# Optimization experiments

Measured on AMD Instinct MI355X. Metric: run time of the kernel, lower is better.

Reference implementation:

```python
import jax, jax.numpy as jnp
import numpy as np

N_NODES = 20000
STEPS = 10  # message_passing_steps


def _mlp(x, p):
    # 3-layer MLP: Linear->ReLU->Linear->ReLU->Linear (no final activation)
    W1, b1, W2, b2, W3, b3 = p
    h = jax.nn.relu(x @ W1 + b1)
    h = jax.nn.relu(h @ W2 + b2)
    return h @ W3 + b3


def _aggregate(dst, edge_attr, num_nodes):
    # scatter_add of edge features into destination nodes, degree-normalized (deg clamped to >=1)
    agg = jax.ops.segment_sum(edge_attr, dst, num_segments=num_nodes)
    deg = jax.ops.segment_sum(jnp.ones((dst.shape[0], 1), edge_attr.dtype), dst, num_segments=num_nodes)
    return agg / jnp.maximum(deg, 1.0)


def setup_inputs() -> dict:
    key = jax.random.key(0)
    N, EM, EC = N_NODES, 120000, 20000
    ND, MD, CD, OD, L = 12, 7, 4, 3, 128
    keys = iter(jax.random.split(key, 128))

    def lin(i, o):
        return (jax.random.normal(next(keys), (i, o), jnp.float32) * 0.05,
                jax.random.normal(next(keys), (o,), jnp.float32) * 0.05)

    inp = {
        "node_x": jax.random.normal(next(keys), (N, ND), jnp.float32),
        "mesh_edge_attr": jax.random.normal(next(keys), (EM, MD), jnp.float32),
        "contact_edge_attr": jax.random.normal(next(keys), (EC, CD), jnp.float32),
    }
    dims = {"ne": (ND, L), "me": (MD, L), "ce": (CD, L), "pe": (3 * L, L), "pn": (3 * L, L), "de": (L, OD)}
    for name, (i, o) in dims.items():
        W1, b1 = lin(i, L)
        W2, b2 = lin(L, L)
        W3, b3 = lin(L, o)
        for pn, p in zip(["W1", "b1", "W2", "b2", "W3", "b3"], [W1, b1, W2, b2, W3, b3]):
            inp[name + "_" + pn] = p
    inp["mesh_edge_index"] = jax.random.randint(next(keys), (2, EM), 0, N)
    inp["contact_edge_index"] = jax.random.randint(next(keys), (2, EC), 0, N)
    return inp


def reference(node_x, mesh_edge_attr, contact_edge_attr,
              ne_W1, ne_b1, ne_W2, ne_b2, ne_W3, ne_b3,
              me_W1, me_b1, me_W2, me_b2, me_W3, me_b3,
              ce_W1, ce_b1, ce_W2, ce_b2, ce_W3, ce_b3,
              pe_W1, pe_b1, pe_W2, pe_b2, pe_W3, pe_b3,
              pn_W1, pn_b1, pn_W2, pn_b2, pn_W3, pn_b3,
              de_W1, de_b1, de_W2, de_b2, de_W3, de_b3,
              mesh_edge_index, contact_edge_index):
    ne = (ne_W1, ne_b1, ne_W2, ne_b2, ne_W3, ne_b3)
    mep = (me_W1, me_b1, me_W2, me_b2, me_W3, me_b3)
    cep = (ce_W1, ce_b1, ce_W2, ce_b2, ce_W3, ce_b3)
    pe = (pe_W1, pe_b1, pe_W2, pe_b2, pe_W3, pe_b3)
    pn = (pn_W1, pn_b1, pn_W2, pn_b2, pn_W3, pn_b3)
    de = (de_W1, de_b1, de_W2, de_b2, de_W3, de_b3)
    N = node_x.shape[0]
    # encode
    x = _mlp(node_x, ne)                 # [N, 128]
    me = _mlp(mesh_edge_attr, mep)       # [EM, 128]
    ce = _mlp(contact_edge_attr, cep)    # [EC, 128]
    msrc, mdst = mesh_edge_index[0], mesh_edge_index[1]
    csrc, cdst = contact_edge_index[0], contact_edge_index[1]
    # process (shared edge_mlp for both edge types, residual updates)
    for _ in range(STEPS):
        me = me + _mlp(jnp.concatenate([x[msrc], x[mdst], me], axis=-1), pe)
        ce = ce + _mlp(jnp.concatenate([x[csrc], x[cdst], ce], axis=-1), pe)
        agg_m = _aggregate(mdst, me, N)
        agg_c = _aggregate(cdst, ce, N)
        x = x + _mlp(jnp.concatenate([x, agg_m, agg_c], axis=-1), pn)
    # decode
    return _mlp(x, de)                   # [N, 3]
```

## Files before the change

### kernel.cpp

```cpp
#include <hip/hip_runtime.h>
#include <stdint.h>

typedef unsigned short u16;
typedef __attribute__((ext_vector_type(8))) short bf16x8;
typedef __attribute__((ext_vector_type(4))) float f32x4;

#define NNODES 20000
#define EM 120000
#define EC 20000
#define LDIM 128
#define MT 32
#define MT2 64
#define A_STR 392
#define H_STR 136
#define G_STR 264

__device__ __forceinline__ u16 f2bf(float f){
  uint32_t b = __float_as_uint(f);
  b += 0x7FFF + ((b >> 16) & 1);
  return (u16)(b >> 16);
}

__device__ __forceinline__ f32x4 mfma16(bf16x8 a, bf16x8 b, f32x4 c){
  return __builtin_amdgcn_mfma_f32_16x16x32_bf16(a, b, c, 0, 0, 0);
}

template<int KB>
__device__ __forceinline__ void layer(const u16* sIn, int in_str, const u16* Wp,
                                      int wr, int wc, int lane, f32x4 acc[4]){
  const int row = wr*16 + (lane & 15);
  const int kg  = lane >> 4;
  #pragma unroll
  for (int kb = 0; kb < KB; ++kb){
    bf16x8 a = *(const bf16x8*)(sIn + row*in_str + kb*32 + kg*8);
    const u16* wb = Wp + (((kb*8 + wc*4)*64 + lane) << 3);
    #pragma unroll
    for (int nf = 0; nf < 4; ++nf){
      bf16x8 b = *(const bf16x8*)(wb + (nf << 9));
      acc[nf] = mfma16(a, b, acc[nf]);
    }
  }
}

__device__ __forceinline__ void hid_epi(f32x4 acc[4], const float* bias,
                                        int wr, int wc, int lane, u16* sOut){
  const int cl = lane & 15;
  const int r0 = wr*16 + (lane >> 4)*4;
  #pragma unroll
  for (int nf = 0; nf < 4; ++nf){
    int col = wc*64 + nf*16 + cl;
    float bv = bias[col];
    #pragma unroll
    for (int r = 0; r < 4; ++r){
      float v = acc[nf][r] + bv;
      sOut[(r0 + r)*H_STR + col] = f2bf(v > 0.f ? v : 0.f);
    }
  }
}

__device__ __forceinline__ void zero4(f32x4 acc[4]){
  const f32x4 vz = {0.f, 0.f, 0.f, 0.f};
  #pragma unroll
  for (int i = 0; i < 4; ++i) acc[i] = vz;
}

template<int KB, int STR>
__device__ __forceinline__ void layer64(const u16* sIn, const u16* Wp,
                                        int wr, int wc, int lane, f32x4 acc[2][2]){
  const int r0 = wr*32 + (lane & 15);
  const int kg = lane >> 4;
  const u16* a0p = sIn + r0*STR + kg*8;
  const u16* a1p = a0p + 16*STR;
  const u16* wb  = Wp + (((wc*2)*64 + lane) << 3);
  #pragma unroll
  for (int kb = 0; kb < KB; ++kb){
    bf16x8 a0 = *(const bf16x8*)(a0p + kb*32);
    bf16x8 a1 = *(const bf16x8*)(a1p + kb*32);
    const u16* wk = wb + kb*4096;
    bf16x8 b0 = *(const bf16x8*)(wk);
    bf16x8 b1 = *(const bf16x8*)(wk + 512);
    acc[0][0] = mfma16(a0, b0, acc[0][0]);
    acc[1][0] = mfma16(a1, b0, acc[1][0]);
    acc[0][1] = mfma16(a0, b1, acc[0][1]);
    acc[1][1] = mfma16(a1, b1, acc[1][1]);
  }
}

template<int STR>
__device__ __forceinline__ void hid_epi64(f32x4 acc[2][2], const float* bias,
                                          int wr, int wc, int lane, u16* sOut){
  const int cl = lane & 15;
  const int rq = (lane >> 4)*4;
  #pragma unroll
  for (int rf = 0; rf < 2; ++rf){
    int r0 = wr*32 + rf*16 + rq;
    #pragma unroll
    for (int nf = 0; nf < 2; ++nf){
      int col = wc*32 + nf*16 + cl;
      float bv = bias[col];
      #pragma unroll
      for (int r = 0; r < 4; ++r){
        float v = acc[rf][nf][r] + bv;
        sOut[(r0 + r)*STR + col] = f2bf(v > 0.f ? v : 0.f);
      }
    }
  }
}

__device__ __forceinline__ void zero22(f32x4 acc[2][2]){
  const f32x4 vz = {0.f, 0.f, 0.f, 0.f};
  acc[0][0] = vz; acc[0][1] = vz; acc[1][0] = vz; acc[1][1] = vz;
}

struct PackDesc { const float* src; int K_raw, N_raw, NF, elem_off; };
struct PackArgs { PackDesc d[18]; int total; };

__global__ __launch_bounds__(256) void pack_weights(PackArgs pa, u16* dst){
  int idx = blockIdx.x*256 + threadIdx.x;
  if (idx >= pa.total) return;
  int di = 0;
  #pragma unroll
  for (int i = 1; i < 18; ++i) if (idx >= pa.d[i].elem_off) di = i;
  PackDesc dd = pa.d[di];
  int e = idx - dd.elem_off;
  int f = e >> 9, lane = (e >> 3) & 63, j = e & 7;
  int kb = f / dd.NF, nf = f % dd.NF;
  int k = kb*32 + (lane >> 4)*8 + j;
  int n = nf*16 + (lane & 15);
  float v = (k < dd.K_raw && n < dd.N_raw) ? dd.src[k*dd.N_raw + n] : 0.f;
  dst[idx] = f2bf(v);
}

__global__ __launch_bounds__(256) void hist_kernel(const int* mdst, const int* cdst,
                                                   int* cnt_m, int* cnt_c){
  int i = blockIdx.x*256 + threadIdx.x;
  if (i < EM) atomicAdd(&cnt_m[mdst[i]], 1);
  else if (i < EM + EC) atomicAdd(&cnt_c[cdst[i - EM]], 1);
}

struct ScanArgs { const int *cnt_m, *cnt_c; int *start_m, *start_c, *cur_m, *cur_c; };

__global__ __launch_bounds__(256) void scan_kernel(ScanArgs a){
  const int n = NNODES;
  const int* cnt = blockIdx.x == 0 ? a.cnt_m : a.cnt_c;
  int* start     = blockIdx.x == 0 ? a.start_m : a.start_c;
  int* cur       = blockIdx.x == 0 ? a.cur_m : a.cur_c;
  __shared__ int part[256];
  __shared__ int base[257];
  int t = threadIdx.x;
  const int per = (n + 255) / 256;
  int lo = t*per, hi = min(n, lo + per);
  int s = 0;
  for (int j = lo; j < hi; ++j) s += cnt[j];
  part[t] = s;
  __syncthreads();
  if (t == 0){
    int run = 0;
    for (int i = 0; i < 256; ++i){ base[i] = run; run += part[i]; }
    base[256] = run;
  }
  __syncthreads();
  int run = base[t];
  for (int j = lo; j < hi; ++j){ start[j] = run; cur[j] = run; run += cnt[j]; }
  if (t == 255) start[n] = base[256];
}

__global__ __launch_bounds__(256) void scatter_kernel(const int* mdst, const int* cdst,
                                                      int* cur_m, int* cur_c,
                                                      int* eid_m, int* eid_c){
  int i = blockIdx.x*256 + threadIdx.x;
  if (i < EM){
    int p = atomicAdd(&cur_m[mdst[i]], 1);
    eid_m[p] = i;
  } else if (i < EM + EC){
    int e = i - EM;
    int p = atomicAdd(&cur_c[cdst[e]], 1);
    eid_c[p] = e;
  }
}

struct EncArgs {
  const float* in; int Kraw;
  const u16 *Wp1, *Wp2, *Wp3;
  const float *b1, *b2, *b3;
  float* out_f32; u16* out_b16;
};

__global__ __launch_bounds__(256) void enc_kernel(EncArgs a){
  __shared__ u16 sA[MT*A_STR];
  __shared__ u16 sH[MT*H_STR];
  const int tid = threadIdx.x, lane = tid & 63, w = tid >> 6, wr = w & 1, wc = w >> 1;
  const int m0 = blockIdx.x * MT;
  for (int i = tid; i < MT*32; i += 256){
    int row = i >> 5, c = i & 31;
    float v = (c < a.Kraw) ? a.in[(size_t)(m0 + row)*a.Kraw + c] : 0.f;
    sA[row*A_STR + c] = f2bf(v);
  }
  __syncthreads();
  f32x4 acc[4]; zero4(acc);
  layer<1>(sA, A_STR, a.Wp1, wr, wc, lane, acc);
  hid_epi(acc, a.b1, wr, wc, lane, sH);
  __syncthreads();
  zero4(acc);
  layer<4>(sH, H_STR, a.Wp2, wr, wc, lane, acc);
  hid_epi(acc, a.b2, wr, wc, lane, sA);
  __syncthreads();
  zero4(acc);
  layer<4>(sA, H_STR, a.Wp3, wr, wc, lane, acc);
  const int cl = lane & 15, r0l = wr*16 + (lane >> 4)*4;
  #pragma unroll
  for (int nf = 0; nf < 4; ++nf){
    int col = wc*64 + nf*16 + cl;
    float bv = a.b3[col];
    #pragma unroll
    for (int r = 0; r < 4; ++r){
      int m = m0 + r0l + r;
      float v = acc[nf][r] + bv;
      a.out_f32[(size_t)m*LDIM + col] = v;
      if (a.out_b16) a.out_b16[(size_t)m*LDIM + col] = f2bf(v);
    }
  }
}

struct EdgeArgs {
  const u16 *Wp1, *Wp2, *Wp3;
  const float *b1, *b2, *b3;
  const u16* x_b16;
  const int *msrc, *mdst, *csrc, *cdst;
  float *me_f32, *ce_f32;
  int mesh_blocks;
};

__global__ __launch_bounds__(512, 8) void edge_kernel(EdgeArgs a){
  __shared__ u16 sB0[MT2*H_STR];
  __shared__ u16 sB1[MT2*H_STR];
  const int tid = threadIdx.x, lane = tid & 63, w = tid >> 6, wr = w & 1, wc = w >> 1;
  const bool mesh = (int)blockIdx.x < a.mesh_blocks;
  const int e0 = (mesh ? (int)blockIdx.x : (int)blockIdx.x - a.mesh_blocks) * MT2;
  const int E = mesh ? EM : EC;
  const int* src = mesh ? a.msrc : a.csrc;
  const int* dst = mesh ? a.mdst : a.cdst;
  float* ff = mesh ? a.me_f32 : a.ce_f32;

  const int r0 = wr*32 + (lane & 15);
  int eA = e0 + r0;      if (eA >= E) eA = E - 1;
  int eB = e0 + r0 + 16; if (eB >= E) eB = E - 1;
  const int sA_ = src[eA], sB_ = src[eB], dA_ = dst[eA], dB_ = dst[eB];

  #pragma unroll
  for (int t = tid; t < MT2*16; t += 512){
    int row = t >> 4, ch = t & 15;
    int e = e0 + row; if (e >= E) e = E - 1;
    const float* sp = ff + (size_t)e*LDIM + ch*8;
    bf16x8 v;
    #pragma unroll
    for (int j = 0; j < 8; ++j) v[j] = (short)f2bf(sp[j]);
    *(bf16x8*)(sB0 + row*H_STR + ch*8) = v;
  }
  __syncthreads();

  f32x4 acc[2][2]; zero22(acc);
  {
    const int cb = (lane >> 4)*8;
    const u16* wb = a.Wp1 + (((wc*2)*64 + lane) << 3);
    #pragma unroll
    for (int kb = 0; kb < 12; ++kb){
      bf16x8 a0, a1;
      if (kb < 4){
        a0 = *(const bf16x8*)(a.x_b16 + (size_t)sA_*LDIM + kb*32 + cb);
        a1 = *(const bf16x8*)(a.x_b16 + (size_t)sB_*LDIM + kb*32 + cb);
      } else if (kb < 8){
        a0 = *(const bf16x8*)(a.x_b16 + (size_t)dA_*LDIM + (kb-4)*32 + cb);
        a1 = *(const bf16x8*)(a.x_b16 + (size_t)dB_*LDIM + (kb-4)*32 + cb);
      } else {
        a0 = *(const bf16x8*)(sB0 + r0*H_STR + (kb-8)*32 + cb);
        a1 = *(const bf16x8*)(sB0 + (r0+16)*H_STR + (kb-8)*32 + cb);
      }
      const u16* wk = wb + kb*4096;
      bf16x8 b0 = *(const bf16x8*)(wk);
      bf16x8 b1 = *(const bf16x8*)(wk + 512);
      acc[0][0] = mfma16(a0, b0, acc[0][0]);
      acc[1][0] = mfma16(a1, b0, acc[1][0]);
      acc[0][1] = mfma16(a0, b1, acc[0][1]);
      acc[1][1] = mfma16(a1, b1, acc[1][1]);
    }
  }
  __syncthreads();
  hid_epi64<H_STR>(acc, a.b1, wr, wc, lane, sB1);
  __syncthreads();
  zero22(acc);
  layer64<4, H_STR>(sB1, a.Wp2, wr, wc, lane, acc);
  hid_epi64<H_STR>(acc, a.b2, wr, wc, lane, sB0);
  __syncthreads();
  zero22(acc);
  layer64<4, H_STR>(sB0, a.Wp3, wr, wc, lane, acc);

  const int cl = lane & 15, rq = (lane >> 4)*4;
  #pragma unroll
  for (int rf = 0; rf < 2; ++rf){
    #pragma unroll
    for (int r = 0; r < 4; ++r){
      int e = e0 + wr*32 + rf*16 + rq + r;
      if (e < E){
        #pragma unroll
        for (int nf = 0; nf < 2; ++nf){
          int col = wc*32 + nf*16 + cl;
          float nv = ff[(size_t)e*LDIM + col] + acc[rf][nf][r] + a.b3[col];
          ff[(size_t)e*LDIM + col] = nv;
        }
      }
    }
  }
}

struct NodeArgs {
  const u16 *Wp1, *Wp2, *Wp3;
  const float *b1, *b2, *b3;
  const u16* x_b16_in;
  const float *me_f32, *ce_f32;
  const int *start_m, *eid_m, *start_c, *eid_c;
  float* x_f32; u16* x_b16_out;
};

__global__ __launch_bounds__(512, 8) void node_kernel(NodeArgs a){
  __shared__ u16 sG[MT2*G_STR];
  const int tid = threadIdx.x, lane = tid & 63, w = tid >> 6, wr = w & 1, wc = w >> 1;
  const int n0 = blockIdx.x * MT2;

  {
    const int r = tid >> 3, c0 = (tid & 7) * 16;
    const int n = n0 + r;
    const bool ok = n < NNODES;
    {
      int s = ok ? a.start_m[n] : 0, e = ok ? a.start_m[n+1] : 0;
      f32x4 a0{0,0,0,0}, a1{0,0,0,0}, a2{0,0,0,0}, a3{0,0,0,0};
      for (int j = s; j < e; ++j){
        const f32x4* p = (const f32x4*)(a.me_f32 + (size_t)a.eid_m[j]*LDIM + c0);
        a0 += p[0]; a1 += p[1]; a2 += p[2]; a3 += p[3];
      }
      float inv = 1.f / fmaxf((float)(e - s), 1.f);
      bf16x8 t0, t1;
      #pragma unroll
      for (int k = 0; k < 4; ++k){
        t0[k]   = (short)f2bf(a0[k]*inv); t0[k+4] = (short)f2bf(a1[k]*inv);
        t1[k]   = (short)f2bf(a2[k]*inv); t1[k+4] = (short)f2bf(a3[k]*inv);
      }
      *(bf16x8*)(sG + r*G_STR + c0) = t0;
      *(bf16x8*)(sG + r*G_STR + c0 + 8) = t1;
    }
    {
      int s = ok ? a.start_c[n] : 0, e = ok ? a.start_c[n+1] : 0;
      f32x4 a0{0,0,0,0}, a1{0,0,0,0}, a2{0,0,0,0}, a3{0,0,0,0};
      for (int j = s; j < e; ++j){
        const f32x4* p = (const f32x4*)(a.ce_f32 + (size_t)a.eid_c[j]*LDIM + c0);
        a0 += p[0]; a1 += p[1]; a2 += p[2]; a3 += p[3];
      }
      float inv = 1.f / fmaxf((float)(e - s), 1.f);
      bf16x8 t0, t1;
      #pragma unroll
      for (int k = 0; k < 4; ++k){
        t0[k]   = (short)f2bf(a0[k]*inv); t0[k+4] = (short)f2bf(a1[k]*inv);
        t1[k]   = (short)f2bf(a2[k]*inv); t1[k+4] = (short)f2bf(a3[k]*inv);
      }
      *(bf16x8*)(sG + r*G_STR + 128 + c0) = t0;
      *(bf16x8*)(sG + r*G_STR + 128 + c0 + 8) = t1;
    }
  }
  __syncthreads();

  const int r0 = wr*32 + (lane & 15);
  int nA = n0 + r0;      if (nA >= NNODES) nA = NNODES - 1;
  int nB = n0 + r0 + 16; if (nB >= NNODES) nB = NNODES - 1;

  f32x4 acc[2][2]; zero22(acc);
  {
    const int cb = (lane >> 4)*8;
    const u16* wb = a.Wp1 + (((wc*2)*64 + lane) << 3);
    #pragma unroll
    for (int kb = 0; kb < 12; ++kb){
      bf16x8 a0, a1;
      if (kb < 4){
        a0 = *(const bf16x8*)(a.x_b16_in + (size_t)nA*LDIM + kb*32 + cb);
        a1 = *(const bf16x8*)(a.x_b16_in + (size_t)nB*LDIM + kb*32 + cb);
      } else {
        a0 = *(const bf16x8*)(sG + r0*G_STR + (kb-4)*32 + cb);
        a1 = *(const bf16x8*)(sG + (r0+16)*G_STR + (kb-4)*32 + cb);
      }
      const u16* wk = wb + kb*4096;
      bf16x8 b0 = *(const bf16x8*)(wk);
      bf16x8 b1 = *(const bf16x8*)(wk + 512);
      acc[0][0] = mfma16(a0, b0, acc[0][0]);
      acc[1][0] = mfma16(a1, b0, acc[1][0]);
      acc[0][1] = mfma16(a0, b1, acc[0][1]);
      acc[1][1] = mfma16(a1, b1, acc[1][1]);
    }
  }
  __syncthreads();
  hid_epi64<G_STR>(acc, a.b1, wr, wc, lane, sG);
  __syncthreads();
  zero22(acc);
  layer64<4, G_STR>(sG, a.Wp2, wr, wc, lane, acc);
  hid_epi64<G_STR>(acc, a.b2, wr, wc, lane, sG + 128);
  __syncthreads();
  zero22(acc);
  layer64<4, G_STR>(sG + 128, a.Wp3, wr, wc, lane, acc);

  const int cl = lane & 15, rq = (lane >> 4)*4;
  #pragma unroll
  for (int rf = 0; rf < 2; ++rf){
    #pragma unroll
    for (int r = 0; r < 4; ++r){
      int n = n0 + wr*32 + rf*16 + rq + r;
      if (n < NNODES){
        #pragma unroll
        for (int nf = 0; nf < 2; ++nf){
          int col = wc*32 + nf*16 + cl;
          float nv = a.x_f32[(size_t)n*LDIM + col] + acc[rf][nf][r] + a.b3[col];
          a.x_f32[(size_t)n*LDIM + col] = nv;
          a.x_b16_out[(size_t)n*LDIM + col] = f2bf(nv);
        }
      }
    }
  }
}

struct DecArgs {
  const u16 *Wp1, *Wp2, *Wp3;
  const float *b1, *b2, *b3;
  const u16* x_b16; float* out;
};

__global__ __launch_bounds__(256) void dec_kernel(DecArgs a){
  __shared__ u16 sA[MT*A_STR];
  __shared__ u16 sH[MT*H_STR];
  const int tid = threadIdx.x, lane = tid & 63, w = tid >> 6, wr = w & 1, wc = w >> 1;
  const int n0 = blockIdx.x * MT;
  for (int i = tid; i < MT*16; i += 256){
    int row = i >> 4, ch = i & 15;
    *(bf16x8*)(sA + row*H_STR + ch*8) = *(const bf16x8*)(a.x_b16 + (size_t)(n0+row)*LDIM + ch*8);
  }
  __syncthreads();
  f32x4 acc[4]; zero4(acc);
  layer<4>(sA, H_STR, a.Wp1, wr, wc, lane, acc);
  hid_epi(acc, a.b1, wr, wc, lane, sH);
  __syncthreads();
  zero4(acc);
  layer<4>(sH, H_STR, a.Wp2, wr, wc, lane, acc);
  hid_epi(acc, a.b2, wr, wc, lane, sA);
  __syncthreads();
  if (wc == 0){
    f32x4 a3 = {0.f, 0.f, 0.f, 0.f};
    const int row = wr*16 + (lane & 15), kg = lane >> 4;
    #pragma unroll
    for (int kb = 0; kb < 4; ++kb){
      bf16x8 av = *(const bf16x8*)(sA + row*H_STR + kb*32 + kg*8);
      bf16x8 bv = *(const bf16x8*)(a.Wp3 + ((kb*64 + lane) << 3));
      a3 = mfma16(av, bv, a3);
    }
    const int cl = lane & 15, r0l = wr*16 + (lane >> 4)*4;
    if (cl < 3){
      #pragma unroll
      for (int r = 0; r < 4; ++r)
        a.out[(size_t)(n0 + r0l + r)*3 + cl] = a3[r] + a.b3[cl];
    }
  }
}

extern "C" void kernel_launch(void* const* d_in, const int* in_sizes, int n_in,
                              void* d_out, int out_size, void* d_ws, size_t ws_size,
                              hipStream_t stream){
  auto F = [&](int i){ return (const float*)d_in[i]; };
  const float* node_x   = F(0);
  const float* mesh_attr = F(1);
  const float* cont_attr = F(2);
  const int* mei = (const int*)d_in[39];
  const int* cei = (const int*)d_in[40];
  const int *msrc = mei, *mdst = mei + EM, *csrc = cei, *cdst = cei + EC;

  char* ws = (char*)d_ws;
  size_t off = 0;
  auto take = [&](size_t b)->void*{ void* p = ws + off; off += (b + 255) & ~(size_t)255; return p; };
  float* x_f32  = (float*)take((size_t)NNODES*LDIM*4);
  u16*   x_b16  = (u16*)  take((size_t)NNODES*LDIM*2);
  float* me_f32 = (float*)take((size_t)EM*LDIM*4);
  float* ce_f32 = (float*)take((size_t)EC*LDIM*4);
  u16*   wpack  = (u16*)  take((size_t)309248*2);
  int* cnt_m   = (int*)take((size_t)NNODES*4);
  int* cnt_c   = (int*)take((size_t)NNODES*4);
  int* start_m = (int*)take((size_t)(NNODES+1)*4);
  int* start_c = (int*)take((size_t)(NNODES+1)*4);
  int* cur_m   = (int*)take((size_t)NNODES*4);
  int* cur_c   = (int*)take((size_t)NNODES*4);
  int* eid_m   = (int*)take((size_t)EM*4);
  int* eid_c   = (int*)take((size_t)EC*4);

  static const int tbl[18][5] = {
    {3,12,128,32,128},{5,128,128,128,128},{7,128,128,128,128},
    {9,7,128,32,128},{11,128,128,128,128},{13,128,128,128,128},
    {15,4,128,32,128},{17,128,128,128,128},{19,128,128,128,128},
    {21,384,128,384,128},{23,128,128,128,128},{25,128,128,128,128},
    {27,384,128,384,128},{29,128,128,128,128},{31,128,128,128,128},
    {33,128,128,128,128},{35,128,128,128,128},{37,128,3,128,16}};
  PackArgs pa; int eo = 0; int offs[18];
  for (int i = 0; i < 18; ++i){
    offs[i] = eo;
    pa.d[i].src = F(tbl[i][0]);
    pa.d[i].K_raw = tbl[i][1];
    pa.d[i].N_raw = tbl[i][2];
    pa.d[i].NF = tbl[i][4] / 16;
    pa.d[i].elem_off = eo;
    eo += tbl[i][3] * tbl[i][4];
  }
  pa.total = eo;
  pack_weights<<<dim3(eo/256), dim3(256), 0, stream>>>(pa, wpack);

  size_t cnt_span = ((char*)cnt_c - (char*)cnt_m) + (size_t)NNODES*4;
  hipMemsetAsync(cnt_m, 0, cnt_span, stream);
  hist_kernel<<<dim3((EM + EC + 255)/256), dim3(256), 0, stream>>>(mdst, cdst, cnt_m, cnt_c);
  ScanArgs sa{cnt_m, cnt_c, start_m, start_c, cur_m, cur_c};
  scan_kernel<<<dim3(2), dim3(256), 0, stream>>>(sa);
  scatter_kernel<<<dim3((EM + EC + 255)/256), dim3(256), 0, stream>>>(mdst, cdst, cur_m, cur_c, eid_m, eid_c);

  EncArgs en{node_x, 12, wpack+offs[0], wpack+offs[1], wpack+offs[2], F(4), F(6), F(8), x_f32, x_b16};
  enc_kernel<<<dim3(NNODES/MT), dim3(256), 0, stream>>>(en);
  EncArgs em{mesh_attr, 7, wpack+offs[3], wpack+offs[4], wpack+offs[5], F(10), F(12), F(14), me_f32, nullptr};
  enc_kernel<<<dim3(EM/MT), dim3(256), 0, stream>>>(em);
  EncArgs ec{cont_attr, 4, wpack+offs[6], wpack+offs[7], wpack+offs[8], F(16), F(18), F(20), ce_f32, nullptr};
  enc_kernel<<<dim3(EC/MT), dim3(256), 0, stream>>>(ec);

  EdgeArgs ea;
  ea.Wp1 = wpack+offs[9]; ea.Wp2 = wpack+offs[10]; ea.Wp3 = wpack+offs[11];
  ea.b1 = F(22); ea.b2 = F(24); ea.b3 = F(26);
  ea.x_b16 = x_b16;
  ea.msrc = msrc; ea.mdst = mdst; ea.csrc = csrc; ea.cdst = cdst;
  ea.me_f32 = me_f32; ea.ce_f32 = ce_f32;
  ea.mesh_blocks = EM/MT2;

  NodeArgs na;
  na.Wp1 = wpack+offs[12]; na.Wp2 = wpack+offs[13]; na.Wp3 = wpack+offs[14];
  na.b1 = F(28); na.b2 = F(30); na.b3 = F(32);
  na.x_b16_in = x_b16;
  na.me_f32 = me_f32; na.ce_f32 = ce_f32;
  na.start_m = start_m; na.eid_m = eid_m; na.start_c = start_c; na.eid_c = eid_c;
  na.x_f32 = x_f32; na.x_b16_out = x_b16;

  const int edge_blocks = EM/MT2 + (EC + MT2 - 1)/MT2;
  const int node_blocks = (NNODES + MT2 - 1)/MT2;
  for (int s = 0; s < 10; ++s){
    edge_kernel<<<dim3(edge_blocks), dim3(512), 0, stream>>>(ea);
    node_kernel<<<dim3(node_blocks), dim3(512), 0, stream>>>(na);
  }

  DecArgs da{wpack+offs[15], wpack+offs[16], wpack+offs[17], F(34), F(36), F(38), x_b16, (float*)d_out};
  dec_kernel<<<dim3(NNODES/MT), dim3(256), 0, stream>>>(da);
}
```

Baseline: 1.345 ms.

## Stage gathered edge inputs in shared memory and vectorize residual writeback

The edge kernel now gathers the src/dst node rows into one concatenated shared tile together with the bf16 copy of the edge state, and runs the first layer from shared memory. Before, each lane issued per-k scattered global loads inside the MFMA loop. The edge's fp32 state is held in registers, and the final output is staged through shared memory so the residual update is written with coalesced float4 stores instead of strided scalar read-modify-write. The larger shared buffer lowers the occupancy hint from 8 to 6 blocks.

```diff
diff --git a/kernel.cpp b/kernel.cpp
--- a/kernel.cpp
+++ b/kernel.cpp
@@ -14,6 +14,7 @@
 #define A_STR 392
 #define H_STR 136
 #define G_STR 264
+#define D_STR 132
 
 __device__ __forceinline__ u16 f2bf(float f){
   uint32_t b = __float_as_uint(f);
@@ -231,9 +232,8 @@
   int mesh_blocks;
 };
 
-__global__ __launch_bounds__(512, 8) void edge_kernel(EdgeArgs a){
-  __shared__ u16 sB0[MT2*H_STR];
-  __shared__ u16 sB1[MT2*H_STR];
+__global__ __launch_bounds__(512, 6) void edge_kernel(EdgeArgs a){
+  __shared__ u16 sCat[MT2*A_STR];
   const int tid = threadIdx.x, lane = tid & 63, w = tid >> 6, wr = w & 1, wc = w >> 1;
   const bool mesh = (int)blockIdx.x < a.mesh_blocks;
   const int e0 = (mesh ? (int)blockIdx.x : (int)blockIdx.x - a.mesh_blocks) * MT2;
@@ -242,74 +242,64 @@
   const int* dst = mesh ? a.mdst : a.cdst;
   float* ff = mesh ? a.me_f32 : a.ce_f32;
 
-  const int r0 = wr*32 + (lane & 15);
-  int eA = e0 + r0;      if (eA >= E) eA = E - 1;
-  int eB = e0 + r0 + 16; if (eB >= E) eB = E - 1;
-  const int sA_ = src[eA], sB_ = src[eB], dA_ = dst[eA], dB_ = dst[eB];
-
-  #pragma unroll
-  for (int t = tid; t < MT2*16; t += 512){
-    int row = t >> 4, ch = t & 15;
+  #pragma unroll
+  for (int i = tid; i < MT2*32; i += 512){
+    int row = i >> 5, c = i & 31;
     int e = e0 + row; if (e >= E) e = E - 1;
-    const float* sp = ff + (size_t)e*LDIM + ch*8;
-    bf16x8 v;
-    #pragma unroll
-    for (int j = 0; j < 8; ++j) v[j] = (short)f2bf(sp[j]);
-    *(bf16x8*)(sB0 + row*H_STR + ch*8) = v;
+    const u16* sp = (c < 16) ? a.x_b16 + (size_t)src[e]*LDIM + c*8
+                             : a.x_b16 + (size_t)dst[e]*LDIM + (c-16)*8;
+    *(bf16x8*)(sCat + row*A_STR + c*8) = *(const bf16x8*)sp;
+  }
+  const int srow = tid >> 3, sj = tid & 7;
+  int se = e0 + srow; if (se >= E) se = E - 1;
+  const f32x4* fp = (const f32x4*)(ff + (size_t)se*LDIM + sj*16);
+  f32x4 p0 = fp[0], p1 = fp[1], p2 = fp[2], p3 = fp[3];
+  {
+    bf16x8 t0, t1;
+    #pragma unroll
+    for (int k = 0; k < 4; ++k){
+      t0[k] = (short)f2bf(p0[k]); t0[k+4] = (short)f2bf(p1[k]);
+      t1[k] = (short)f2bf(p2[k]); t1[k+4] = (short)f2bf(p3[k]);
+    }
+    *(bf16x8*)(sCat + srow*A_STR + 256 + sj*16) = t0;
+    *(bf16x8*)(sCat + srow*A_STR + 256 + sj*16 + 8) = t1;
   }
   __syncthreads();
 
   f32x4 acc[2][2]; zero22(acc);
+  layer64<12, A_STR>(sCat, a.Wp1, wr, wc, lane, acc);
+  __syncthreads();
+  hid_epi64<A_STR>(acc, a.b1, wr, wc, lane, sCat + 256);
+  __syncthreads();
+  zero22(acc);
+  layer64<4, A_STR>(sCat + 256, a.Wp2, wr, wc, lane, acc);
+  hid_epi64<A_STR>(acc, a.b2, wr, wc, lane, sCat);
+  __syncthreads();
+  zero22(acc);
+  layer64<4, A_STR>(sCat, a.Wp3, wr, wc, lane, acc);
+  __syncthreads();
+
+  float* dd = (float*)sCat;
   {
-    const int cb = (lane >> 4)*8;
-    const u16* wb = a.Wp1 + (((wc*2)*64 + lane) << 3);
-    #pragma unroll
-    for (int kb = 0; kb < 12; ++kb){
-      bf16x8 a0, a1;
-      if (kb < 4){
-        a0 = *(const bf16x8*)(a.x_b16 + (size_t)sA_*LDIM + kb*32 + cb);
-        a1 = *(const bf16x8*)(a.x_b16 + (size_t)sB_*LDIM + kb*32 + cb);
-      } else if (kb < 8){
-        a0 = *(const bf16x8*)(a.x_b16 + (size_t)dA_*LDIM + (kb-4)*32 + cb);
-        a1 = *(const bf16x8*)(a.x_b16 + (size_t)dB_*LDIM + (kb-4)*32 + cb);
-      } else {
-        a0 = *(const bf16x8*)(sB0 + r0*H_STR + (kb-8)*32 + cb);
-        a1 = *(const bf16x8*)(sB0 + (r0+16)*H_STR + (kb-8)*32 + cb);
-      }
-      const u16* wk = wb + kb*4096;
-      bf16x8 b0 = *(const bf16x8*)(wk);
-      bf16x8 b1 = *(const bf16x8*)(wk + 512);
-      acc[0][0] = mfma16(a0, b0, acc[0][0]);
-      acc[1][0] = mfma16(a1, b0, acc[1][0]);
-      acc[0][1] = mfma16(a0, b1, acc[0][1]);
-      acc[1][1] = mfma16(a1, b1, acc[1][1]);
-    }
-  }
-  __syncthreads();
-  hid_epi64<H_STR>(acc, a.b1, wr, wc, lane, sB1);
-  __syncthreads();
-  zero22(acc);
-  layer64<4, H_STR>(sB1, a.Wp2, wr, wc, lane, acc);
-  hid_epi64<H_STR>(acc, a.b2, wr, wc, lane, sB0);
-  __syncthreads();
-  zero22(acc);
-  layer64<4, H_STR>(sB0, a.Wp3, wr, wc, lane, acc);
-
-  const int cl = lane & 15, rq = (lane >> 4)*4;
-  #pragma unroll
-  for (int rf = 0; rf < 2; ++rf){
-    #pragma unroll
-    for (int r = 0; r < 4; ++r){
-      int e = e0 + wr*32 + rf*16 + rq + r;
-      if (e < E){
+    const int cl = lane & 15, rq = (lane >> 4)*4;
+    #pragma unroll
+    for (int rf = 0; rf < 2; ++rf){
+      #pragma unroll
+      for (int nf = 0; nf < 2; ++nf){
+        int col = wc*32 + nf*16 + cl;
+        float bv = a.b3[col];
         #pragma unroll
-        for (int nf = 0; nf < 2; ++nf){
-          int col = wc*32 + nf*16 + cl;
-          float nv = ff[(size_t)e*LDIM + col] + acc[rf][nf][r] + a.b3[col];
-          ff[(size_t)e*LDIM + col] = nv;
-        }
-      }
-    }
+        for (int r = 0; r < 4; ++r)
+          dd[(wr*32 + rf*16 + rq + r)*D_STR + col] = acc[rf][nf][r] + bv;
+      }
+    }
+  }
+  __syncthreads();
+  if (e0 + srow < E){
+    float* op = ff + (size_t)(e0 + srow)*LDIM + sj*16;
+    const f32x4* dp = (const f32x4*)(dd + srow*D_STR + sj*16);
+    f32x4 n0 = p0 + dp[0], n1 = p1 + dp[1], n2 = p2 + dp[2], n3 = p3 + dp[3];
+    ((f32x4*)op)[0] = n0; ((f32x4*)op)[1] = n1; ((f32x4*)op)[2] = n2; ((f32x4*)op)[3] = n3;
   }
 }
 
```

Result: faster. 1.218 ms (-9.4%).
